# Optimization experiments

Hardware: AMD Instinct MI355X
Metric: run time of the kernel (lower is better)

The kernel has to match this reference:

```python
import jax, jax.numpy as jnp
import numpy as np

INPUT_DIM = 1024
HIDDEN_DIM = 64   # per-head dim
NUM_HEADS = 16
PROJ = HIDDEN_DIM * NUM_HEADS  # 1024


def setup_inputs() -> dict:
    key = jax.random.key(0)
    ks = jax.random.split(key, 9)
    s = 1.0 / np.sqrt(INPUT_DIM)
    x = jax.random.normal(ks[0], (4, 2048, INPUT_DIM), dtype=jnp.float32)
    # Linear weights stored [in, out] (math-equivalent to torch's W.T)
    Wq = jax.random.uniform(ks[1], (INPUT_DIM, PROJ), jnp.float32, -s, s)
    bq = jax.random.uniform(ks[2], (PROJ,), jnp.float32, -s, s)
    Wk = jax.random.uniform(ks[3], (INPUT_DIM, PROJ), jnp.float32, -s, s)
    bk = jax.random.uniform(ks[4], (PROJ,), jnp.float32, -s, s)
    Wv = jax.random.uniform(ks[5], (INPUT_DIM, PROJ), jnp.float32, -s, s)
    bv = jax.random.uniform(ks[6], (PROJ,), jnp.float32, -s, s)
    sf = 1.0 / np.sqrt(PROJ)
    Wf = jax.random.uniform(ks[7], (PROJ, HIDDEN_DIM), jnp.float32, -sf, sf)
    bf = jax.random.uniform(ks[8], (HIDDEN_DIM,), jnp.float32, -sf, sf)
    return {"x": x, "Wq": Wq, "bq": bq, "Wk": Wk, "bk": bk,
            "Wv": Wv, "bv": bv, "Wf": Wf, "bf": bf}


def reference(x, Wq, bq, Wk, bk, Wv, bv, Wf, bf):
    B, S, _ = x.shape
    def split_heads(t):  # [B,S,H*D] -> [B,H,S,D]
        return t.reshape(B, S, NUM_HEADS, HIDDEN_DIM).transpose(0, 2, 1, 3)
    q = split_heads(x @ Wq + bq)
    k = split_heads(x @ Wk + bk)
    v = split_heads(x @ Wv + bv)
    scale = 1.0 / jnp.sqrt(jnp.float32(HIDDEN_DIM))
    scores = jnp.einsum('bhqd,bhkd->bhqk', q, k) * scale  # [B,H,S,S]
    weights = jax.nn.softmax(scores, axis=-1)
    ctx = jnp.einsum('bhqk,bhkd->bhqd', weights, v)
    ctx = ctx.transpose(0, 2, 1, 3).reshape(B, S, PROJ)
    return ctx @ Wf + bf  # [B,S,HIDDEN_DIM]
```

## Files before the change

kernel.cpp:

```cpp
#include <hip/hip_runtime.h>
#include <math.h>

#define S_LEN 2048
#define NH 16
#define HD 64
#define DMODEL 1024
#define BATCH 4
#define M_TOT (BATCH * S_LEN)

typedef __attribute__((ext_vector_type(8))) short bf16x8;
typedef __attribute__((ext_vector_type(4))) float f32x4;

#define CK 0.18033688f

__device__ __forceinline__ unsigned short f2bf_rne(float f) {
    unsigned u = __float_as_uint(f);
    u += 0x7fffu + ((u >> 16) & 1u);
    return (unsigned short)(u >> 16);
}

__device__ __forceinline__ void gld16(unsigned short* lds, const unsigned short* g) {
    __builtin_amdgcn_global_load_lds(
        (const __attribute__((address_space(1))) void*)g,
        (__attribute__((address_space(3))) void*)lds, 16, 0, 0);
}

__global__ __launch_bounds__(256) void cvt_x(
    const float* __restrict__ x, unsigned short* __restrict__ xb)
{
    size_t i = ((size_t)blockIdx.x * 256 + threadIdx.x) * 4;
    float4 v = *(const float4*)(x + i);
    unsigned short t[4];
    t[0] = f2bf_rne(v.x); t[1] = f2bf_rne(v.y);
    t[2] = f2bf_rne(v.z); t[3] = f2bf_rne(v.w);
    *(uint2*)(xb + i) = *(uint2*)t;
}

__global__ __launch_bounds__(256) void cvt_wT(
    const float* __restrict__ Wq, const float* __restrict__ Wk,
    const float* __restrict__ Wv, const float* __restrict__ Wf,
    unsigned short* __restrict__ WT)
{
    const int z = blockIdx.z;
    if (z == 3 && blockIdx.x > 0) return;
    const float* W = (z == 0) ? Wq : (z == 1) ? Wk : (z == 2) ? Wv : Wf;
    const int ncol = (z == 3) ? 64 : DMODEL;
    unsigned short* out = WT + (size_t)z * DMODEL * DMODEL;

    __shared__ float Lt[64][65];
    const int tid = threadIdx.x;
    const int r0 = blockIdx.y * 64;
    const int c0 = blockIdx.x * 64;

    #pragma unroll
    for (int p = 0; p < 4; p++) {
        int row = (tid >> 4) + p * 16;
        int c4 = (tid & 15) * 4;
        float4 v = *(const float4*)(W + (size_t)(r0 + row) * ncol + c0 + c4);
        Lt[row][c4 + 0] = v.x; Lt[row][c4 + 1] = v.y;
        Lt[row][c4 + 2] = v.z; Lt[row][c4 + 3] = v.w;
    }
    __syncthreads();
    #pragma unroll
    for (int p = 0; p < 4; p++) {
        int nr = (tid >> 4) + p * 16;
        int kc = (tid & 15) * 4;
        unsigned short t[4];
        #pragma unroll
        for (int j = 0; j < 4; j++) t[j] = f2bf_rne(Lt[kc + j][nr]);
        *(uint2*)(out + (size_t)(c0 + nr) * DMODEL + r0 + kc) = *(uint2*)t;
    }
}

__global__ __launch_bounds__(256) void qkv_gemm_mfma(
    const unsigned short* __restrict__ xb,
    const unsigned short* __restrict__ WT,
    const float* __restrict__ bq, const float* __restrict__ bk,
    const float* __restrict__ bv,
    unsigned short* __restrict__ Qb, unsigned short* __restrict__ Kb,
    unsigned short* __restrict__ Vtb)
{
    __shared__ __align__(16) unsigned short As[16 * 512];
    __shared__ __align__(16) unsigned short Bs[16 * 512];

    const int z = blockIdx.z;
    const unsigned short* Wz = WT + (size_t)z * DMODEL * DMODEL;
    const float* bias = (z == 0) ? bq : (z == 1) ? bk : bv;

    const int tid = threadIdx.x;
    const int lane = tid & 63, w = tid >> 6;
    const int quad = lane >> 4, l15 = lane & 15;
    const int wm = w & 1, wn = w >> 1;

    const int OC0 = blockIdx.x * 128;
    const int R0  = blockIdx.y * 128;

    const unsigned short* gA0 = Wz + (size_t)(OC0 + w * 16 + l15) * DMODEL + quad * 8;
    const unsigned short* gA1 = gA0 + (size_t)64 * DMODEL;
    const unsigned short* gB0 = xb + (size_t)(R0 + w * 16 + l15) * DMODEL + quad * 8;
    const unsigned short* gB1 = gB0 + (size_t)64 * DMODEL;

    f32x4 acc[4][4];
    #pragma unroll
    for (int i = 0; i < 4; i++)
        #pragma unroll
        for (int j = 0; j < 4; j++)
            #pragma unroll
            for (int c = 0; c < 4; c++) acc[i][j][c] = 0.f;

    for (int k0 = 0; k0 < DMODEL; k0 += 64) {
        __syncthreads();
        gld16(As + ((w + 0) * 2 + 0) * 512, gA0 + k0);
        gld16(As + ((w + 0) * 2 + 1) * 512, gA0 + k0 + 32);
        gld16(As + ((w + 4) * 2 + 0) * 512, gA1 + k0);
        gld16(As + ((w + 4) * 2 + 1) * 512, gA1 + k0 + 32);
        gld16(Bs + ((w + 0) * 2 + 0) * 512, gB0 + k0);
        gld16(Bs + ((w + 0) * 2 + 1) * 512, gB0 + k0 + 32);
        gld16(Bs + ((w + 4) * 2 + 0) * 512, gB1 + k0);
        gld16(Bs + ((w + 4) * 2 + 1) * 512, gB1 + k0 + 32);
        __syncthreads();

        #pragma unroll
        for (int sl = 0; sl < 2; sl++) {
            bf16x8 af[4], bfr[4];
            #pragma unroll
            for (int t = 0; t < 4; t++) {
                af[t]  = *(const bf16x8*)&As[((wm * 4 + t) * 2 + sl) * 512 + lane * 8];
                bfr[t] = *(const bf16x8*)&Bs[((wn * 4 + t) * 2 + sl) * 512 + lane * 8];
            }
            if (z != 2) {
                #pragma unroll
                for (int mt = 0; mt < 4; mt++)
                    #pragma unroll
                    for (int nt = 0; nt < 4; nt++)
                        acc[mt][nt] = __builtin_amdgcn_mfma_f32_16x16x32_bf16(
                            af[mt], bfr[nt], acc[mt][nt], 0, 0, 0);
            } else {
                #pragma unroll
                for (int mt = 0; mt < 4; mt++)
                    #pragma unroll
                    for (int nt = 0; nt < 4; nt++)
                        acc[mt][nt] = __builtin_amdgcn_mfma_f32_16x16x32_bf16(
                            bfr[nt], af[mt], acc[mt][nt], 0, 0, 0);
            }
        }
    }

    if (z != 2) {
        unsigned short* out = (z == 0) ? Qb : Kb;
        const float qs = (z == 0) ? CK : 1.0f;
        #pragma unroll
        for (int mt = 0; mt < 4; mt++) {
            int oc = OC0 + wm * 64 + mt * 16 + quad * 4;
            float4 bv4 = *(const float4*)&bias[oc];
            #pragma unroll
            for (int nt = 0; nt < 4; nt++) {
                int row = R0 + wn * 64 + nt * 16 + l15;
                unsigned short t4[4];
                t4[0] = f2bf_rne((acc[mt][nt][0] + bv4.x) * qs);
                t4[1] = f2bf_rne((acc[mt][nt][1] + bv4.y) * qs);
                t4[2] = f2bf_rne((acc[mt][nt][2] + bv4.z) * qs);
                t4[3] = f2bf_rne((acc[mt][nt][3] + bv4.w) * qs);
                *(uint2*)(out + (size_t)row * DMODEL + oc) = *(uint2*)t4;
            }
        }
    } else {
        const int b = R0 >> 11;
        const int sbase = (R0 & 2047) + wn * 64;
        #pragma unroll
        for (int mt = 0; mt < 4; mt++) {
            int oc = OC0 + wm * 64 + mt * 16 + l15;
            float bvv = bias[oc];
            #pragma unroll
            for (int nt = 0; nt < 4; nt++) {
                int s = sbase + nt * 16 + quad * 4;
                unsigned short t4[4];
                t4[0] = f2bf_rne(acc[mt][nt][0] + bvv);
                t4[1] = f2bf_rne(acc[mt][nt][1] + bvv);
                t4[2] = f2bf_rne(acc[mt][nt][2] + bvv);
                t4[3] = f2bf_rne(acc[mt][nt][3] + bvv);
                *(uint2*)(Vtb + (size_t)(b * DMODEL + oc) * S_LEN + s) = *(uint2*)t4;
            }
        }
    }
}

__global__ __launch_bounds__(256, 4) void flash_attn_mfma(
    const unsigned short* __restrict__ Qg,
    const unsigned short* __restrict__ Kg,
    const unsigned short* __restrict__ Vtg,
    unsigned short* __restrict__ ctxb)
{
    __shared__ __align__(16) unsigned short Ks[16 * 512];
    __shared__ __align__(16) unsigned short Vs[16 * 512];
    __shared__ __align__(16) unsigned short Ps[8 * 512];

    const int tid  = threadIdx.x;
    const int lane = tid & 63, w = tid >> 6;
    const int quad = lane >> 4, l15 = lane & 15;
    const int b = blockIdx.z, h = blockIdx.y;
    const int r0 = blockIdx.x * 128;

    bf16x8 qf[2][2];
    #pragma unroll
    for (int nt = 0; nt < 2; nt++)
        #pragma unroll
        for (int ds = 0; ds < 2; ds++)
            qf[nt][ds] = *(const bf16x8*)(Qg +
                (size_t)(b * S_LEN + r0 + w * 32 + nt * 16 + l15) * DMODEL +
                h * HD + ds * 32 + quad * 8);

    const unsigned short* gK = Kg + (size_t)(b * S_LEN + w * 16 + l15) * DMODEL + h * HD + quad * 8;
    const unsigned short* gV = Vtg + ((size_t)((b * NH + h) * HD + w * 16 + l15)) * S_LEN + quad * 8;

    f32x4 O[2][4], lsum[2];
    #pragma unroll
    for (int rt = 0; rt < 2; rt++) {
        #pragma unroll
        for (int c = 0; c < 4; c++) lsum[rt][c] = 0.f;
        #pragma unroll
        for (int dt = 0; dt < 4; dt++)
            #pragma unroll
            for (int c = 0; c < 4; c++) O[rt][dt][c] = 0.f;
    }

    f32x4 zero4;
    #pragma unroll
    for (int c = 0; c < 4; c++) zero4[c] = 0.f;
    bf16x8 ones;
    #pragma unroll
    for (int c = 0; c < 8; c++) ones[c] = (short)0x3F80;

    for (int st = 0; st < S_LEN / 128; st++) {
        __syncthreads();
        gld16(Ks + ((w + 0) * 2 + 0) * 512, gK);
        gld16(Ks + ((w + 0) * 2 + 1) * 512, gK + 32);
        gld16(Ks + ((w + 4) * 2 + 0) * 512, gK + (size_t)64 * DMODEL);
        gld16(Ks + ((w + 4) * 2 + 1) * 512, gK + (size_t)64 * DMODEL + 32);
        gld16(Vs + (w * 4 + 0) * 512, gV);
        gld16(Vs + (w * 4 + 1) * 512, gV + 32);
        gld16(Vs + (w * 4 + 2) * 512, gV + 64);
        gld16(Vs + (w * 4 + 3) * 512, gV + 96);
        gK += (size_t)128 * DMODEL;
        gV += 128;
        __syncthreads();

        #pragma unroll
        for (int r = 0; r < 4; r++) {
            f32x4 sc[2][2];
            {
                bf16x8 kf0 = *(const bf16x8*)&Ks[((r * 2 + 0) * 2 + 0) * 512 + lane * 8];
                bf16x8 kf1 = *(const bf16x8*)&Ks[((r * 2 + 1) * 2 + 0) * 512 + lane * 8];
                sc[0][0] = __builtin_amdgcn_mfma_f32_16x16x32_bf16(kf0, qf[0][0], zero4, 0, 0, 0);
                sc[0][1] = __builtin_amdgcn_mfma_f32_16x16x32_bf16(kf0, qf[1][0], zero4, 0, 0, 0);
                sc[1][0] = __builtin_amdgcn_mfma_f32_16x16x32_bf16(kf1, qf[0][0], zero4, 0, 0, 0);
                sc[1][1] = __builtin_amdgcn_mfma_f32_16x16x32_bf16(kf1, qf[1][0], zero4, 0, 0, 0);
                kf0 = *(const bf16x8*)&Ks[((r * 2 + 0) * 2 + 1) * 512 + lane * 8];
                kf1 = *(const bf16x8*)&Ks[((r * 2 + 1) * 2 + 1) * 512 + lane * 8];
                sc[0][0] = __builtin_amdgcn_mfma_f32_16x16x32_bf16(kf0, qf[0][1], sc[0][0], 0, 0, 0);
                sc[0][1] = __builtin_amdgcn_mfma_f32_16x16x32_bf16(kf0, qf[1][1], sc[0][1], 0, 0, 0);
                sc[1][0] = __builtin_amdgcn_mfma_f32_16x16x32_bf16(kf1, qf[0][1], sc[1][0], 0, 0, 0);
                sc[1][1] = __builtin_amdgcn_mfma_f32_16x16x32_bf16(kf1, qf[1][1], sc[1][1], 0, 0, 0);
            }

            #pragma unroll
            for (int nt = 0; nt < 2; nt++) {
                #pragma unroll
                for (int mt = 0; mt < 2; mt++) {
                    unsigned u[4];
                    #pragma unroll
                    for (int c = 0; c < 4; c++)
                        u[c] = __float_as_uint(exp2f(sc[mt][nt][c]));
                    uint2 pk;
                    pk.x = __builtin_amdgcn_perm(u[1], u[0], 0x07060302u);
                    pk.y = __builtin_amdgcn_perm(u[3], u[2], 0x07060302u);
                    int off = (w * 2 + nt) * 512 + (mt * 2 + (quad >> 1)) * 128 +
                              l15 * 8 + (quad & 1) * 4;
                    *(uint2*)&Ps[off] = pk;
                }
            }

            bf16x8 pf0 = *(const bf16x8*)&Ps[(w * 2 + 0) * 512 + lane * 8];
            bf16x8 pf1 = *(const bf16x8*)&Ps[(w * 2 + 1) * 512 + lane * 8];
            lsum[0] = __builtin_amdgcn_mfma_f32_16x16x32_bf16(pf0, ones, lsum[0], 0, 0, 0);
            lsum[1] = __builtin_amdgcn_mfma_f32_16x16x32_bf16(pf1, ones, lsum[1], 0, 0, 0);
            #pragma unroll
            for (int dt = 0; dt < 4; dt++) {
                bf16x8 vf = *(const bf16x8*)&Vs[(dt * 4 + r) * 512 + lane * 8];
                O[0][dt] = __builtin_amdgcn_mfma_f32_16x16x32_bf16(pf0, vf, O[0][dt], 0, 0, 0);
                O[1][dt] = __builtin_amdgcn_mfma_f32_16x16x32_bf16(pf1, vf, O[1][dt], 0, 0, 0);
            }
        }
    }

    const size_t srow = (size_t)(b * S_LEN + r0 + w * 32);
    #pragma unroll
    for (int rt = 0; rt < 2; rt++) {
        #pragma unroll
        for (int reg = 0; reg < 4; reg++) {
            float li = 1.0f / lsum[rt][reg];
            size_t rowoff = (srow + rt * 16 + quad * 4 + reg) * DMODEL + h * HD + l15;
            #pragma unroll
            for (int dt = 0; dt < 4; dt++)
                ctxb[rowoff + dt * 16] = f2bf_rne(O[rt][dt][reg] * li);
        }
    }
}

__global__ __launch_bounds__(256) void out_proj_mfma(
    const unsigned short* __restrict__ ctxb,
    const unsigned short* __restrict__ WfT,
    const float* __restrict__ bfb,
    float* __restrict__ out)
{
    __shared__ float Red[4 * 1024];

    const int tid = threadIdx.x;
    const int lane = tid & 63, w = tid >> 6;
    const int quad = lane >> 4, l15 = lane & 15;
    const int m0 = blockIdx.x * 16;

    const unsigned short* pA = ctxb + (size_t)(m0 + l15) * DMODEL + w * 256 + quad * 8;
    const unsigned short* pB = WfT + (size_t)l15 * DMODEL + w * 256 + quad * 8;

    f32x4 acc[4];
    #pragma unroll
    for (int j = 0; j < 4; j++)
        #pragma unroll
        for (int c = 0; c < 4; c++) acc[j][c] = 0.f;

    #pragma unroll
    for (int k0 = 0; k0 < 256; k0 += 32) {
        bf16x8 af = *(const bf16x8*)(pA + k0);
        #pragma unroll
        for (int j = 0; j < 4; j++) {
            bf16x8 bfr = *(const bf16x8*)(pB + (size_t)j * 16 * DMODEL + k0);
            acc[j] = __builtin_amdgcn_mfma_f32_16x16x32_bf16(af, bfr, acc[j], 0, 0, 0);
        }
    }

    #pragma unroll
    for (int j = 0; j < 4; j++)
        #pragma unroll
        for (int reg = 0; reg < 4; reg++)
            Red[w * 1024 + lane * 16 + j * 4 + reg] = acc[j][reg];
    __syncthreads();

    const int row  = tid >> 4;
    const int col4 = (tid & 15) * 4;
    const int j    = col4 >> 4;
    float4 o;
    float* op = &o.x;
    #pragma unroll
    for (int cc = 0; cc < 4; cc++) {
        int rl = (row >> 2) * 16 + ((col4 + cc) & 15);
        int idx = rl * 16 + j * 4 + (row & 3);
        float s = Red[idx] + Red[1024 + idx] + Red[2048 + idx] + Red[3072 + idx];
        op[cc] = s + bfb[col4 + cc];
    }
    *(float4*)(out + (size_t)(m0 + row) * HD + col4) = o;
}

extern "C" void kernel_launch(void* const* d_in, const int* in_sizes, int n_in,
                              void* d_out, int out_size, void* d_ws, size_t ws_size,
                              hipStream_t stream)
{
    (void)in_sizes; (void)n_in; (void)out_size; (void)ws_size;
    const float* x  = (const float*)d_in[0];
    const float* Wq = (const float*)d_in[1];
    const float* bq = (const float*)d_in[2];
    const float* Wk = (const float*)d_in[3];
    const float* bk = (const float*)d_in[4];
    const float* Wv = (const float*)d_in[5];
    const float* bv = (const float*)d_in[6];
    const float* Wf = (const float*)d_in[7];
    const float* bf = (const float*)d_in[8];
    float* out = (float*)d_out;

    char* wsb = (char*)d_ws;
    unsigned short* xb   = (unsigned short*)wsb;
    unsigned short* ctxb = (unsigned short*)wsb;
    unsigned short* WT   = xb + (size_t)M_TOT * DMODEL;
    unsigned short* WfT  = WT + (size_t)3 * DMODEL * DMODEL;
    unsigned short* Qb   = (unsigned short*)(wsb + (size_t)32 * 1024 * 1024);
    unsigned short* Kb   = Qb + (size_t)M_TOT * DMODEL;
    unsigned short* Vtb  = Kb + (size_t)M_TOT * DMODEL;

    cvt_x<<<dim3(M_TOT * DMODEL / 4 / 256), 256, 0, stream>>>(x, xb);
    cvt_wT<<<dim3(16, 16, 4), 256, 0, stream>>>(Wq, Wk, Wv, Wf, WT);
    qkv_gemm_mfma<<<dim3(8, 64, 3), 256, 0, stream>>>(xb, WT, bq, bk, bv, Qb, Kb, Vtb);
    flash_attn_mfma<<<dim3(S_LEN / 128, NH, BATCH), 256, 0, stream>>>(Qb, Kb, Vtb, ctxb);
    out_proj_mfma<<<dim3(M_TOT / 16), 256, 0, stream>>>(ctxb, WfT, bf, out);
}
```

Measured before the change: 311.8 us.

## Shrink attention query tile to 64 rows and split out-proj K across 8 waves

The flash attention kernel now processes 64 query rows per block (16 per wave) with 64-key tiles, halving the LDS buffers and per-wave accumulators and raising the occupancy hint to 6 blocks per CU. It also switches to the raw hardware exp2 builtin. The output projection uses 512 threads, each wave covering 128 of the K dimension, with an 8-way LDS reduction. The aim is more parallelism and occupancy, at the cost of less K/V reuse per loaded tile (twice the global K/V traffic) and more barriers per unit of work.

```diff
diff --git a/kernel.cpp b/kernel.cpp
--- a/kernel.cpp
+++ b/kernel.cpp
@@ -185,44 +185,39 @@
     }
 }
 
-__global__ __launch_bounds__(256, 4) void flash_attn_mfma(
+__global__ __launch_bounds__(256, 6) void flash_attn_mfma(
     const unsigned short* __restrict__ Qg,
     const unsigned short* __restrict__ Kg,
     const unsigned short* __restrict__ Vtg,
     unsigned short* __restrict__ ctxb)
 {
-    __shared__ __align__(16) unsigned short Ks[16 * 512];
-    __shared__ __align__(16) unsigned short Vs[16 * 512];
-    __shared__ __align__(16) unsigned short Ps[8 * 512];
+    __shared__ __align__(16) unsigned short Ks[8 * 512];
+    __shared__ __align__(16) unsigned short Vs[8 * 512];
+    __shared__ __align__(16) unsigned short Ps[4 * 512];
 
     const int tid  = threadIdx.x;
     const int lane = tid & 63, w = tid >> 6;
     const int quad = lane >> 4, l15 = lane & 15;
     const int b = blockIdx.z, h = blockIdx.y;
-    const int r0 = blockIdx.x * 128;
-
-    bf16x8 qf[2][2];
-    #pragma unroll
-    for (int nt = 0; nt < 2; nt++)
-        #pragma unroll
-        for (int ds = 0; ds < 2; ds++)
-            qf[nt][ds] = *(const bf16x8*)(Qg +
-                (size_t)(b * S_LEN + r0 + w * 32 + nt * 16 + l15) * DMODEL +
-                h * HD + ds * 32 + quad * 8);
+    const int r0 = blockIdx.x * 64;
+
+    bf16x8 qf[2];
+    #pragma unroll
+    for (int ds = 0; ds < 2; ds++)
+        qf[ds] = *(const bf16x8*)(Qg +
+            (size_t)(b * S_LEN + r0 + w * 16 + l15) * DMODEL +
+            h * HD + ds * 32 + quad * 8);
 
     const unsigned short* gK = Kg + (size_t)(b * S_LEN + w * 16 + l15) * DMODEL + h * HD + quad * 8;
     const unsigned short* gV = Vtg + ((size_t)((b * NH + h) * HD + w * 16 + l15)) * S_LEN + quad * 8;
 
-    f32x4 O[2][4], lsum[2];
-    #pragma unroll
-    for (int rt = 0; rt < 2; rt++) {
-        #pragma unroll
-        for (int c = 0; c < 4; c++) lsum[rt][c] = 0.f;
-        #pragma unroll
-        for (int dt = 0; dt < 4; dt++)
-            #pragma unroll
-            for (int c = 0; c < 4; c++) O[rt][dt][c] = 0.f;
-    }
+    f32x4 O[4], lsum;
+    #pragma unroll
+    for (int c = 0; c < 4; c++) lsum[c] = 0.f;
+    #pragma unroll
+    for (int dt = 0; dt < 4; dt++)
+        #pragma unroll
+        for (int c = 0; c < 4; c++) O[dt][c] = 0.f;
 
     f32x4 zero4;
     #pragma unroll
@@ -231,97 +226,71 @@
     #pragma unroll
     for (int c = 0; c < 8; c++) ones[c] = (short)0x3F80;
 
-    for (int st = 0; st < S_LEN / 128; st++) {
+    for (int st = 0; st < S_LEN / 64; st++) {
         __syncthreads();
-        gld16(Ks + ((w + 0) * 2 + 0) * 512, gK);
-        gld16(Ks + ((w + 0) * 2 + 1) * 512, gK + 32);
-        gld16(Ks + ((w + 4) * 2 + 0) * 512, gK + (size_t)64 * DMODEL);
-        gld16(Ks + ((w + 4) * 2 + 1) * 512, gK + (size_t)64 * DMODEL + 32);
-        gld16(Vs + (w * 4 + 0) * 512, gV);
-        gld16(Vs + (w * 4 + 1) * 512, gV + 32);
-        gld16(Vs + (w * 4 + 2) * 512, gV + 64);
-        gld16(Vs + (w * 4 + 3) * 512, gV + 96);
-        gK += (size_t)128 * DMODEL;
-        gV += 128;
+        gld16(Ks + (w * 2 + 0) * 512, gK);
+        gld16(Ks + (w * 2 + 1) * 512, gK + 32);
+        gld16(Vs + (w * 2 + 0) * 512, gV);
+        gld16(Vs + (w * 2 + 1) * 512, gV + 32);
+        gK += (size_t)64 * DMODEL;
+        gV += 64;
         __syncthreads();
 
         #pragma unroll
-        for (int r = 0; r < 4; r++) {
-            f32x4 sc[2][2];
-            {
-                bf16x8 kf0 = *(const bf16x8*)&Ks[((r * 2 + 0) * 2 + 0) * 512 + lane * 8];
-                bf16x8 kf1 = *(const bf16x8*)&Ks[((r * 2 + 1) * 2 + 0) * 512 + lane * 8];
-                sc[0][0] = __builtin_amdgcn_mfma_f32_16x16x32_bf16(kf0, qf[0][0], zero4, 0, 0, 0);
-                sc[0][1] = __builtin_amdgcn_mfma_f32_16x16x32_bf16(kf0, qf[1][0], zero4, 0, 0, 0);
-                sc[1][0] = __builtin_amdgcn_mfma_f32_16x16x32_bf16(kf1, qf[0][0], zero4, 0, 0, 0);
-                sc[1][1] = __builtin_amdgcn_mfma_f32_16x16x32_bf16(kf1, qf[1][0], zero4, 0, 0, 0);
-                kf0 = *(const bf16x8*)&Ks[((r * 2 + 0) * 2 + 1) * 512 + lane * 8];
-                kf1 = *(const bf16x8*)&Ks[((r * 2 + 1) * 2 + 1) * 512 + lane * 8];
-                sc[0][0] = __builtin_amdgcn_mfma_f32_16x16x32_bf16(kf0, qf[0][1], sc[0][0], 0, 0, 0);
-                sc[0][1] = __builtin_amdgcn_mfma_f32_16x16x32_bf16(kf0, qf[1][1], sc[0][1], 0, 0, 0);
-                sc[1][0] = __builtin_amdgcn_mfma_f32_16x16x32_bf16(kf1, qf[0][1], sc[1][0], 0, 0, 0);
-                sc[1][1] = __builtin_amdgcn_mfma_f32_16x16x32_bf16(kf1, qf[1][1], sc[1][1], 0, 0, 0);
-            }
-
-            #pragma unroll
-            for (int nt = 0; nt < 2; nt++) {
+        for (int r = 0; r < 2; r++) {
+            #pragma unroll
+            for (int mt = 0; mt < 2; mt++) {
+                bf16x8 kf0 = *(const bf16x8*)&Ks[((r * 2 + mt) * 2 + 0) * 512 + lane * 8];
+                bf16x8 kf1 = *(const bf16x8*)&Ks[((r * 2 + mt) * 2 + 1) * 512 + lane * 8];
+                f32x4 sc = __builtin_amdgcn_mfma_f32_16x16x32_bf16(kf0, qf[0], zero4, 0, 0, 0);
+                sc = __builtin_amdgcn_mfma_f32_16x16x32_bf16(kf1, qf[1], sc, 0, 0, 0);
+                unsigned u[4];
                 #pragma unroll
-                for (int mt = 0; mt < 2; mt++) {
-                    unsigned u[4];
-                    #pragma unroll
-                    for (int c = 0; c < 4; c++)
-                        u[c] = __float_as_uint(exp2f(sc[mt][nt][c]));
-                    uint2 pk;
-                    pk.x = __builtin_amdgcn_perm(u[1], u[0], 0x07060302u);
-                    pk.y = __builtin_amdgcn_perm(u[3], u[2], 0x07060302u);
-                    int off = (w * 2 + nt) * 512 + (mt * 2 + (quad >> 1)) * 128 +
-                              l15 * 8 + (quad & 1) * 4;
-                    *(uint2*)&Ps[off] = pk;
-                }
-            }
-
-            bf16x8 pf0 = *(const bf16x8*)&Ps[(w * 2 + 0) * 512 + lane * 8];
-            bf16x8 pf1 = *(const bf16x8*)&Ps[(w * 2 + 1) * 512 + lane * 8];
-            lsum[0] = __builtin_amdgcn_mfma_f32_16x16x32_bf16(pf0, ones, lsum[0], 0, 0, 0);
-            lsum[1] = __builtin_amdgcn_mfma_f32_16x16x32_bf16(pf1, ones, lsum[1], 0, 0, 0);
+                for (int c = 0; c < 4; c++)
+                    u[c] = __float_as_uint(__builtin_amdgcn_exp2f(sc[c]));
+                uint2 pk;
+                pk.x = __builtin_amdgcn_perm(u[1], u[0], 0x07060302u);
+                pk.y = __builtin_amdgcn_perm(u[3], u[2], 0x07060302u);
+                int off = w * 512 + (mt * 2 + (quad >> 1)) * 128 + l15 * 8 + (quad & 1) * 4;
+                *(uint2*)&Ps[off] = pk;
+            }
+
+            bf16x8 pf = *(const bf16x8*)&Ps[w * 512 + lane * 8];
+            lsum = __builtin_amdgcn_mfma_f32_16x16x32_bf16(pf, ones, lsum, 0, 0, 0);
             #pragma unroll
             for (int dt = 0; dt < 4; dt++) {
-                bf16x8 vf = *(const bf16x8*)&Vs[(dt * 4 + r) * 512 + lane * 8];
-                O[0][dt] = __builtin_amdgcn_mfma_f32_16x16x32_bf16(pf0, vf, O[0][dt], 0, 0, 0);
-                O[1][dt] = __builtin_amdgcn_mfma_f32_16x16x32_bf16(pf1, vf, O[1][dt], 0, 0, 0);
-            }
-        }
-    }
-
-    const size_t srow = (size_t)(b * S_LEN + r0 + w * 32);
-    #pragma unroll
-    for (int rt = 0; rt < 2; rt++) {
-        #pragma unroll
-        for (int reg = 0; reg < 4; reg++) {
-            float li = 1.0f / lsum[rt][reg];
-            size_t rowoff = (srow + rt * 16 + quad * 4 + reg) * DMODEL + h * HD + l15;
-            #pragma unroll
-            for (int dt = 0; dt < 4; dt++)
-                ctxb[rowoff + dt * 16] = f2bf_rne(O[rt][dt][reg] * li);
-        }
-    }
-}
-
-__global__ __launch_bounds__(256) void out_proj_mfma(
+                bf16x8 vf = *(const bf16x8*)&Vs[(dt * 2 + r) * 512 + lane * 8];
+                O[dt] = __builtin_amdgcn_mfma_f32_16x16x32_bf16(pf, vf, O[dt], 0, 0, 0);
+            }
+        }
+    }
+
+    const size_t qbase = (size_t)(b * S_LEN + r0 + w * 16 + quad * 4);
+    #pragma unroll
+    for (int reg = 0; reg < 4; reg++) {
+        float li = 1.0f / lsum[reg];
+        size_t rowoff = (qbase + reg) * DMODEL + h * HD + l15;
+        #pragma unroll
+        for (int dt = 0; dt < 4; dt++)
+            ctxb[rowoff + dt * 16] = f2bf_rne(O[dt][reg] * li);
+    }
+}
+
+__global__ __launch_bounds__(512) void out_proj_mfma(
     const unsigned short* __restrict__ ctxb,
     const unsigned short* __restrict__ WfT,
     const float* __restrict__ bfb,
     float* __restrict__ out)
 {
-    __shared__ float Red[4 * 1024];
+    __shared__ float Red[8 * 1024];
 
     const int tid = threadIdx.x;
     const int lane = tid & 63, w = tid >> 6;
     const int quad = lane >> 4, l15 = lane & 15;
     const int m0 = blockIdx.x * 16;
 
-    const unsigned short* pA = ctxb + (size_t)(m0 + l15) * DMODEL + w * 256 + quad * 8;
-    const unsigned short* pB = WfT + (size_t)l15 * DMODEL + w * 256 + quad * 8;
+    const unsigned short* pA = ctxb + (size_t)(m0 + l15) * DMODEL + w * 128 + quad * 8;
+    const unsigned short* pB = WfT + (size_t)l15 * DMODEL + w * 128 + quad * 8;
 
     f32x4 acc[4];
     #pragma unroll
@@ -330,7 +299,7 @@
         for (int c = 0; c < 4; c++) acc[j][c] = 0.f;
 
     #pragma unroll
-    for (int k0 = 0; k0 < 256; k0 += 32) {
+    for (int k0 = 0; k0 < 128; k0 += 32) {
         bf16x8 af = *(const bf16x8*)(pA + k0);
         #pragma unroll
         for (int j = 0; j < 4; j++) {
@@ -346,19 +315,20 @@
             Red[w * 1024 + lane * 16 + j * 4 + reg] = acc[j][reg];
     __syncthreads();
 
-    const int row  = tid >> 4;
-    const int col4 = (tid & 15) * 4;
-    const int j    = col4 >> 4;
-    float4 o;
+    const int row = tid >> 5;
+    const int c0  = (tid & 31) * 2;
+    float2 o;
     float* op = &o.x;
     #pragma unroll
-    for (int cc = 0; cc < 4; cc++) {
-        int rl = (row >> 2) * 16 + ((col4 + cc) & 15);
-        int idx = rl * 16 + j * 4 + (row & 3);
-        float s = Red[idx] + Red[1024 + idx] + Red[2048 + idx] + Red[3072 + idx];
-        op[cc] = s + bfb[col4 + cc];
-    }
-    *(float4*)(out + (size_t)(m0 + row) * HD + col4) = o;
+    for (int cc = 0; cc < 2; cc++) {
+        int col = c0 + cc;
+        int idx = ((row >> 2) * 16 + (col & 15)) * 16 + (col >> 4) * 4 + (row & 3);
+        float s = 0.f;
+        #pragma unroll
+        for (int wv = 0; wv < 8; wv++) s += Red[wv * 1024 + idx];
+        op[cc] = s + bfb[col];
+    }
+    *(float2*)(out + (size_t)(m0 + row) * HD + c0) = o;
 }
 
 extern "C" void kernel_launch(void* const* d_in, const int* in_sizes, int n_in,
@@ -389,6 +359,6 @@
     cvt_x<<<dim3(M_TOT * DMODEL / 4 / 256), 256, 0, stream>>>(x, xb);
     cvt_wT<<<dim3(16, 16, 4), 256, 0, stream>>>(Wq, Wk, Wv, Wf, WT);
     qkv_gemm_mfma<<<dim3(8, 64, 3), 256, 0, stream>>>(xb, WT, bq, bk, bv, Qb, Kb, Vtb);
-    flash_attn_mfma<<<dim3(S_LEN / 128, NH, BATCH), 256, 0, stream>>>(Qb, Kb, Vtb, ctxb);
-    out_proj_mfma<<<dim3(M_TOT / 16), 256, 0, stream>>>(ctxb, WfT, bf, out);
-}
+    flash_attn_mfma<<<dim3(S_LEN / 64, NH, BATCH), 256, 0, stream>>>(Qb, Kb, Vtb, ctxb);
+    out_proj_mfma<<<dim3(M_TOT / 16), 512, 0, stream>>>(ctxb, WfT, bf, out);
+}
```

Result: slower. 337.9 us (+8.4%).
